# Performance work log

Measured on AMD Instinct MI355X. Metric: run time of the kernel, lower is better.

## Reference

```python
import jax, jax.numpy as jnp
import numpy as np


def setup_inputs() -> dict:
    key = jax.random.key(0)
    k1, k2 = jax.random.split(key)
    B, H = 128, 1024
    log_alpha = jax.random.normal(k1, (B, H), dtype=jnp.float32)
    unnormalized_tran = jax.random.normal(k2, (H, H), dtype=jnp.float32)
    return {"log_alpha": log_alpha, "unnormalized_tran": unnormalized_tran}


def reference(log_alpha, unnormalized_tran):
    # tran[i, j] = log P(state j | state i), rows normalized in log space
    tran = jax.nn.log_softmax(unnormalized_tran, axis=-1)  # (H, H)
    # log-domain matmul: out[b, j] = logsumexp_i(log_alpha[b, i] + tran[i, j])
    # broadcast to (B, H, H) then reduce over the source-state axis i
    out = jax.scipy.special.logsumexp(
        log_alpha[:, :, None] + tran[None, :, :], axis=1
    )  # (B, H)
    return out
```

## Files before the change

### kernel.cpp

```cpp
#include <hip/hip_runtime.h>
#include <hip/hip_bf16.h>

#define H 1024
#define B 128

typedef unsigned short u16;
typedef unsigned int u32;
typedef __attribute__((ext_vector_type(8))) short bf16x8;
typedef __attribute__((ext_vector_type(4))) float f32x4;

static __device__ inline u16 f2bf(float x) {
    __hip_bfloat16 h = __float2bfloat16(x);
    return __builtin_bit_cast(u16, h);
}

__global__ __launch_bounds__(256) void k1(const float* __restrict__ A,
                                          const float* __restrict__ U,
                                          u16* __restrict__ expUP,
                                          u16* __restrict__ expA) {
    const int t = threadIdx.x, w = t >> 6, l = t & 63;
    const int blk = blockIdx.x;
    if (blk < 128) {
        __shared__ u16 Lq[8][1024];
        #pragma unroll
        for (int rr = 0; rr < 2; ++rr) {
            const int row = w * 2 + rr;
            const float* Ur = U + (size_t)(blk * 8 + row) * H;
            float e[16];
            float s = 0.f;
            #pragma unroll
            for (int c = 0; c < 4; ++c) {
                float4 u4 = *reinterpret_cast<const float4*>(Ur + c * 256 + l * 4);
                e[c*4+0] = __expf(u4.x); e[c*4+1] = __expf(u4.y);
                e[c*4+2] = __expf(u4.z); e[c*4+3] = __expf(u4.w);
                s += e[c*4+0] + e[c*4+1] + e[c*4+2] + e[c*4+3];
            }
            #pragma unroll
            for (int off = 32; off > 0; off >>= 1) s += __shfl_down(s, off, 64);
            const float is = 1.0f / __shfl(s, 0, 64);
            #pragma unroll
            for (int c = 0; c < 4; ++c) {
                ushort4 o = {f2bf(e[c*4+0]*is), f2bf(e[c*4+1]*is),
                             f2bf(e[c*4+2]*is), f2bf(e[c*4+3]*is)};
                *reinterpret_cast<ushort4*>(&Lq[row][c*256 + l*4]) = o;
            }
        }
        __syncthreads();
        u16* dst = expUP + (size_t)blk * (H * 8);
        #pragma unroll
        for (int c = 0; c < 4; ++c) {
            const int j = c * 256 + t;
            uint4 v;
            v.x = (u32)Lq[0][j] | ((u32)Lq[1][j] << 16);
            v.y = (u32)Lq[2][j] | ((u32)Lq[3][j] << 16);
            v.z = (u32)Lq[4][j] | ((u32)Lq[5][j] << 16);
            v.w = (u32)Lq[6][j] | ((u32)Lq[7][j] << 16);
            *reinterpret_cast<uint4*>(dst + (size_t)j * 8) = v;
        }
    } else {
        const int b = (blk - 128) * 4 + w;
        const float* Ar = A + (size_t)b * H;
        u16* Er = expA + (size_t)b * H;
        #pragma unroll
        for (int c = 0; c < 4; ++c) {
            float4 a4 = *reinterpret_cast<const float4*>(Ar + c * 256 + l * 4);
            ushort4 o = {f2bf(__expf(a4.x)), f2bf(__expf(a4.y)),
                         f2bf(__expf(a4.z)), f2bf(__expf(a4.w))};
            *reinterpret_cast<ushort4*>(Er + c * 256 + l * 4) = o;
        }
    }
}

__global__ __launch_bounds__(512) void k2(const u16* __restrict__ expA,
                                          const u16* __restrict__ expUP,
                                          float* __restrict__ out) {
    __shared__ float red[4][2][4][66];
    const int t = threadIdx.x, l = t & 63, w = t >> 6;
    const int jh = w & 1, kh = w >> 1;
    const int b0 = blockIdx.x * 16;
    const int j0 = blockIdx.y * 32;
    const int colJ = j0 + jh * 16 + (l & 15);
    const int arow = b0 + (l & 15);
    const int kg   = l >> 4;

    f32x4 acc = {0.f, 0.f, 0.f, 0.f};
    #pragma unroll
    for (int s = 0; s < 8; ++s) {
        const int kk = s * 128 + kh * 32 + kg * 8;
        bf16x8 af = *reinterpret_cast<const bf16x8*>(expA + (size_t)arow * H + kk);
        bf16x8 bfv = *reinterpret_cast<const bf16x8*>(expUP + ((size_t)(kk >> 3) * H + colJ) * 8);
        acc = __builtin_amdgcn_mfma_f32_16x16x32_bf16(af, bfv, acc, 0, 0, 0);
    }

    #pragma unroll
    for (int r = 0; r < 4; ++r) red[kh][jh][r][l] = acc[r];
    __syncthreads();

    const int row = t >> 5, c = t & 31;
    const int jj = c >> 4, cc = c & 15;
    const int ll = (row >> 2) * 16 + cc, r = row & 3;
    const float v = red[0][jj][r][ll] + red[1][jj][r][ll]
                  + red[2][jj][r][ll] + red[3][jj][r][ll];
    out[(size_t)(b0 + row) * H + j0 + c] = __logf(v);
}

extern "C" void kernel_launch(void* const* d_in, const int* in_sizes, int n_in,
                              void* d_out, int out_size, void* d_ws, size_t ws_size,
                              hipStream_t stream) {
    const float* A = (const float*)d_in[0];
    const float* U = (const float*)d_in[1];
    float* out = (float*)d_out;

    char* ws = (char*)d_ws;
    u16* expUP = (u16*)ws;
    u16* expA  = (u16*)(ws + (size_t)2 * 1024 * 1024);

    k1<<<160, 256, 0, stream>>>(A, U, expUP, expA);
    dim3 g(B / 16, H / 32);
    k2<<<g, 512, 0, stream>>>(expA, expUP, out);
}
```

Before: 14.01 us.

## Repack transition matrix in 4-row groups and split work across more blocks

k1 now processes 4 rows of U per block across 256 blocks, using cross-wave shared-memory partial sums instead of an 8-row LDS transpose. The packed layout becomes 4 rows per column, so k2 loads two uint2 pieces per MFMA operand. k2 uses 16-column tiles with all 8 waves splitting K, which doubles the grid to 512 blocks and raises parallelism. In exchange it adds narrower, less coalesced loads and an 8-way reduction per output.

Result: slower. 15.17 us (+8.2%).

```diff
diff --git a/kernel.cpp b/kernel.cpp
--- a/kernel.cpp
+++ b/kernel.cpp
@@ -13,95 +13,104 @@
     __hip_bfloat16 h = __float2bfloat16(x);
     return __builtin_bit_cast(u16, h);
 }
+static __device__ inline u32 pack2(u16 a, u16 b) { return (u32)a | ((u32)b << 16); }
 
 __global__ __launch_bounds__(256) void k1(const float* __restrict__ A,
                                           const float* __restrict__ U,
-                                          u16* __restrict__ expUP,
+                                          u16* __restrict__ expUP4,
                                           u16* __restrict__ expA) {
     const int t = threadIdx.x, w = t >> 6, l = t & 63;
     const int blk = blockIdx.x;
-    if (blk < 128) {
-        __shared__ u16 Lq[8][1024];
+    if (blk < 256) {
+        __shared__ float part[4][4];
+        const int jbase = w * 256 + l;
+        float e[4][4];
+        float p[4] = {0.f, 0.f, 0.f, 0.f};
         #pragma unroll
-        for (int rr = 0; rr < 2; ++rr) {
-            const int row = w * 2 + rr;
-            const float* Ur = U + (size_t)(blk * 8 + row) * H;
-            float e[16];
-            float s = 0.f;
+        for (int r = 0; r < 4; ++r) {
+            const float* Ur = U + (size_t)(blk * 4 + r) * H;
             #pragma unroll
-            for (int c = 0; c < 4; ++c) {
-                float4 u4 = *reinterpret_cast<const float4*>(Ur + c * 256 + l * 4);
-                e[c*4+0] = __expf(u4.x); e[c*4+1] = __expf(u4.y);
-                e[c*4+2] = __expf(u4.z); e[c*4+3] = __expf(u4.w);
-                s += e[c*4+0] + e[c*4+1] + e[c*4+2] + e[c*4+3];
-            }
-            #pragma unroll
-            for (int off = 32; off > 0; off >>= 1) s += __shfl_down(s, off, 64);
-            const float is = 1.0f / __shfl(s, 0, 64);
-            #pragma unroll
-            for (int c = 0; c < 4; ++c) {
-                ushort4 o = {f2bf(e[c*4+0]*is), f2bf(e[c*4+1]*is),
-                             f2bf(e[c*4+2]*is), f2bf(e[c*4+3]*is)};
-                *reinterpret_cast<ushort4*>(&Lq[row][c*256 + l*4]) = o;
+            for (int m = 0; m < 4; ++m) {
+                float v = __expf(Ur[jbase + m * 64]);
+                e[r][m] = v;
+                p[r] += v;
             }
         }
+        #pragma unroll
+        for (int r = 0; r < 4; ++r)
+            #pragma unroll
+            for (int off = 32; off > 0; off >>= 1)
+                p[r] += __shfl_xor(p[r], off, 64);
+        if (l == 0) {
+            #pragma unroll
+            for (int r = 0; r < 4; ++r) part[r][w] = p[r];
+        }
         __syncthreads();
-        u16* dst = expUP + (size_t)blk * (H * 8);
+        float is[4];
         #pragma unroll
-        for (int c = 0; c < 4; ++c) {
-            const int j = c * 256 + t;
-            uint4 v;
-            v.x = (u32)Lq[0][j] | ((u32)Lq[1][j] << 16);
-            v.y = (u32)Lq[2][j] | ((u32)Lq[3][j] << 16);
-            v.z = (u32)Lq[4][j] | ((u32)Lq[5][j] << 16);
-            v.w = (u32)Lq[6][j] | ((u32)Lq[7][j] << 16);
-            *reinterpret_cast<uint4*>(dst + (size_t)j * 8) = v;
+        for (int r = 0; r < 4; ++r)
+            is[r] = 1.0f / (part[r][0] + part[r][1] + part[r][2] + part[r][3]);
+        u16* dst = expUP4 + (size_t)blk * H * 4;
+        #pragma unroll
+        for (int m = 0; m < 4; ++m) {
+            const int j = jbase + m * 64;
+            uint2 v;
+            v.x = pack2(f2bf(e[0][m] * is[0]), f2bf(e[1][m] * is[1]));
+            v.y = pack2(f2bf(e[2][m] * is[2]), f2bf(e[3][m] * is[3]));
+            *reinterpret_cast<uint2*>(dst + (size_t)j * 4) = v;
         }
     } else {
-        const int b = (blk - 128) * 4 + w;
-        const float* Ar = A + (size_t)b * H;
-        u16* Er = expA + (size_t)b * H;
+        const int bb = (blk - 256) * 4;
         #pragma unroll
-        for (int c = 0; c < 4; ++c) {
-            float4 a4 = *reinterpret_cast<const float4*>(Ar + c * 256 + l * 4);
+        for (int r = 0; r < 4; ++r) {
+            const float* Ar = A + (size_t)(bb + r) * H;
+            u16* Er = expA + (size_t)(bb + r) * H;
+            const int j = w * 256 + l * 4;
+            float4 a4 = *reinterpret_cast<const float4*>(Ar + j);
             ushort4 o = {f2bf(__expf(a4.x)), f2bf(__expf(a4.y)),
                          f2bf(__expf(a4.z)), f2bf(__expf(a4.w))};
-            *reinterpret_cast<ushort4*>(Er + c * 256 + l * 4) = o;
+            *reinterpret_cast<ushort4*>(Er + j) = o;
         }
     }
 }
 
 __global__ __launch_bounds__(512) void k2(const u16* __restrict__ expA,
-                                          const u16* __restrict__ expUP,
+                                          const u16* __restrict__ expUP4,
                                           float* __restrict__ out) {
-    __shared__ float red[4][2][4][66];
-    const int t = threadIdx.x, l = t & 63, w = t >> 6;
-    const int jh = w & 1, kh = w >> 1;
+    __shared__ float red[8][4][68];
+    const int t = threadIdx.x, l = t & 63, kh = t >> 6;
     const int b0 = blockIdx.x * 16;
-    const int j0 = blockIdx.y * 32;
-    const int colJ = j0 + jh * 16 + (l & 15);
+    const int j0 = blockIdx.y * 16;
+    const int col  = j0 + (l & 15);
     const int arow = b0 + (l & 15);
     const int kg   = l >> 4;
 
     f32x4 acc = {0.f, 0.f, 0.f, 0.f};
     #pragma unroll
-    for (int s = 0; s < 8; ++s) {
-        const int kk = s * 128 + kh * 32 + kg * 8;
+    for (int s = 0; s < 4; ++s) {
+        const int kk = kh * 128 + s * 32 + kg * 8;
         bf16x8 af = *reinterpret_cast<const bf16x8*>(expA + (size_t)arow * H + kk);
-        bf16x8 bfv = *reinterpret_cast<const bf16x8*>(expUP + ((size_t)(kk >> 3) * H + colJ) * 8);
+        const int kq = kk >> 2;
+        uint2 g0 = *reinterpret_cast<const uint2*>(expUP4 + ((size_t)kq * H + col) * 4);
+        uint2 g1 = *reinterpret_cast<const uint2*>(expUP4 + ((size_t)(kq + 1) * H + col) * 4);
+        uint4 bw = {g0.x, g0.y, g1.x, g1.y};
+        bf16x8 bfv = __builtin_bit_cast(bf16x8, bw);
         acc = __builtin_amdgcn_mfma_f32_16x16x32_bf16(af, bfv, acc, 0, 0, 0);
     }
 
     #pragma unroll
-    for (int r = 0; r < 4; ++r) red[kh][jh][r][l] = acc[r];
+    for (int r = 0; r < 4; ++r) red[kh][r][l] = acc[r];
     __syncthreads();
 
-    const int row = t >> 5, c = t & 31;
-    const int jj = c >> 4, cc = c & 15;
-    const int ll = (row >> 2) * 16 + cc, r = row & 3;
-    const float v = red[0][jj][r][ll] + red[1][jj][r][ll]
-                  + red[2][jj][r][ll] + red[3][jj][r][ll];
-    out[(size_t)(b0 + row) * H + j0 + c] = __logf(v);
+    if (t < 256) {
+        const int row = t >> 4, c = t & 15;
+        const int kg2 = row >> 2, r = row & 3;
+        const int lane = kg2 * 16 + c;
+        float v = 0.f;
+        #pragma unroll
+        for (int k = 0; k < 8; ++k) v += red[k][r][lane];
+        out[(size_t)(b0 + row) * H + j0 + c] = __logf(v);
+    }
 }
 
 extern "C" void kernel_launch(void* const* d_in, const int* in_sizes, int n_in,
@@ -112,10 +121,10 @@
     float* out = (float*)d_out;
 
     char* ws = (char*)d_ws;
-    u16* expUP = (u16*)ws;
-    u16* expA  = (u16*)(ws + (size_t)2 * 1024 * 1024);
+    u16* expUP4 = (u16*)ws;
+    u16* expA   = (u16*)(ws + (size_t)2 * 1024 * 1024);
 
-    k1<<<160, 256, 0, stream>>>(A, U, expUP, expA);
-    dim3 g(B / 16, H / 32);
-    k2<<<g, 512, 0, stream>>>(expA, expUP, out);
+    k1<<<288, 256, 0, stream>>>(A, U, expUP4, expA);
+    dim3 g(B / 16, H / 16);
+    k2<<<g, 512, 0, stream>>>(expA, expUP4, out);
 }
```

## Fold softmax row normalization into exp(A) and compute exp(U) inside matmul

Applied to the files above, without the earlier changes.

The row-wise softmax denominator of the transition matrix is moved onto the A side: k1 now computes only the row sums of exp(U) and writes exp(A[b,k])/sum_k into a bf16 buffer. k2 reads raw U directly and computes exp/bf16 conversion on the fly, so the normalized, repacked exp(U) buffer (2 MB written and re-read) is no longer needed. In exchange, each k2 block recomputes exp of its U tile for every batch tile (8x redundant transcendental work and fp32 U reads), uses strided scalar U loads, and switches the grid order so j-tiles are adjacent.

After: 16.17 us. 1.15x slower.

```diff
diff --git a/kernel.cpp b/kernel.cpp
--- a/kernel.cpp
+++ b/kernel.cpp
@@ -6,6 +6,7 @@
 
 typedef unsigned short u16;
 typedef unsigned int u32;
+typedef unsigned long long u64;
 typedef __attribute__((ext_vector_type(8))) short bf16x8;
 typedef __attribute__((ext_vector_type(4))) float f32x4;
 
@@ -13,72 +14,51 @@
     __hip_bfloat16 h = __float2bfloat16(x);
     return __builtin_bit_cast(u16, h);
 }
+static __device__ inline void st32a(u32* p, u32 v) {
+    __hip_atomic_store(p, v, __ATOMIC_RELAXED, __HIP_MEMORY_SCOPE_AGENT);
+}
+static __device__ inline u64 ld64a(const u16* p) {
+    return __hip_atomic_load((const u64*)p, __ATOMIC_RELAXED, __HIP_MEMORY_SCOPE_AGENT);
+}
 
 __global__ __launch_bounds__(256) void k1(const float* __restrict__ A,
                                           const float* __restrict__ U,
-                                          u16* __restrict__ expUP,
-                                          u16* __restrict__ expA) {
+                                          u16* __restrict__ expAS) {
     const int t = threadIdx.x, w = t >> 6, l = t & 63;
     const int blk = blockIdx.x;
-    if (blk < 128) {
-        __shared__ u16 Lq[8][1024];
-        #pragma unroll
-        for (int rr = 0; rr < 2; ++rr) {
-            const int row = w * 2 + rr;
-            const float* Ur = U + (size_t)(blk * 8 + row) * H;
-            float e[16];
-            float s = 0.f;
-            #pragma unroll
-            for (int c = 0; c < 4; ++c) {
-                float4 u4 = *reinterpret_cast<const float4*>(Ur + c * 256 + l * 4);
-                e[c*4+0] = __expf(u4.x); e[c*4+1] = __expf(u4.y);
-                e[c*4+2] = __expf(u4.z); e[c*4+3] = __expf(u4.w);
-                s += e[c*4+0] + e[c*4+1] + e[c*4+2] + e[c*4+3];
-            }
-            #pragma unroll
-            for (int off = 32; off > 0; off >>= 1) s += __shfl_down(s, off, 64);
-            const float is = 1.0f / __shfl(s, 0, 64);
-            #pragma unroll
-            for (int c = 0; c < 4; ++c) {
-                ushort4 o = {f2bf(e[c*4+0]*is), f2bf(e[c*4+1]*is),
-                             f2bf(e[c*4+2]*is), f2bf(e[c*4+3]*is)};
-                *reinterpret_cast<ushort4*>(&Lq[row][c*256 + l*4]) = o;
-            }
-        }
-        __syncthreads();
-        u16* dst = expUP + (size_t)blk * (H * 8);
+    __shared__ float part[4];
+    {
+        const float* Ur = U + (size_t)(blk * 4 + w) * H;
+        float s = 0.f;
         #pragma unroll
         for (int c = 0; c < 4; ++c) {
-            const int j = c * 256 + t;
-            uint4 v;
-            v.x = (u32)Lq[0][j] | ((u32)Lq[1][j] << 16);
-            v.y = (u32)Lq[2][j] | ((u32)Lq[3][j] << 16);
-            v.z = (u32)Lq[4][j] | ((u32)Lq[5][j] << 16);
-            v.w = (u32)Lq[6][j] | ((u32)Lq[7][j] << 16);
-            *reinterpret_cast<uint4*>(dst + (size_t)j * 8) = v;
+            float4 u4 = *reinterpret_cast<const float4*>(Ur + c * 256 + l * 4);
+            s += __expf(u4.x) + __expf(u4.y) + __expf(u4.z) + __expf(u4.w);
         }
-    } else {
-        const int b = (blk - 128) * 4 + w;
-        const float* Ar = A + (size_t)b * H;
-        u16* Er = expA + (size_t)b * H;
         #pragma unroll
-        for (int c = 0; c < 4; ++c) {
-            float4 a4 = *reinterpret_cast<const float4*>(Ar + c * 256 + l * 4);
-            ushort4 o = {f2bf(__expf(a4.x)), f2bf(__expf(a4.y)),
-                         f2bf(__expf(a4.z)), f2bf(__expf(a4.w))};
-            *reinterpret_cast<ushort4*>(Er + c * 256 + l * 4) = o;
-        }
+        for (int off = 32; off > 0; off >>= 1) s += __shfl_xor(s, off, 64);
+        if (l == 0) part[w] = 1.0f / s;
+    }
+    __syncthreads();
+    {
+        const int b  = t & 127;
+        const int kp = t >> 7;
+        const int k  = blk * 4 + kp * 2;
+        float2 a2 = *reinterpret_cast<const float2*>(A + (size_t)b * H + k);
+        const u32 v = (u32)f2bf(__expf(a2.x) * part[kp * 2])
+                    | ((u32)f2bf(__expf(a2.y) * part[kp * 2 + 1]) << 16);
+        st32a((u32*)(expAS + (size_t)b * H + k), v);
     }
 }
 
-__global__ __launch_bounds__(512) void k2(const u16* __restrict__ expA,
-                                          const u16* __restrict__ expUP,
+__global__ __launch_bounds__(512) void k2(const u16* __restrict__ expAS,
+                                          const float* __restrict__ U,
                                           float* __restrict__ out) {
     __shared__ float red[4][2][4][66];
     const int t = threadIdx.x, l = t & 63, w = t >> 6;
     const int jh = w & 1, kh = w >> 1;
-    const int b0 = blockIdx.x * 16;
-    const int j0 = blockIdx.y * 32;
+    const int j0 = blockIdx.x * 32;
+    const int b0 = blockIdx.y * 16;
     const int colJ = j0 + jh * 16 + (l & 15);
     const int arow = b0 + (l & 15);
     const int kg   = l >> 4;
@@ -87,9 +67,22 @@
     #pragma unroll
     for (int s = 0; s < 8; ++s) {
         const int kk = s * 128 + kh * 32 + kg * 8;
-        bf16x8 af = *reinterpret_cast<const bf16x8*>(expA + (size_t)arow * H + kk);
-        bf16x8 bfv = *reinterpret_cast<const bf16x8*>(expUP + ((size_t)(kk >> 3) * H + colJ) * 8);
-        acc = __builtin_amdgcn_mfma_f32_16x16x32_bf16(af, bfv, acc, 0, 0, 0);
+        const u16* ap = expAS + (size_t)arow * H + kk;
+        const u64 alo = ld64a(ap), ahi = ld64a(ap + 4);
+        const float* up = U + (size_t)kk * H + colJ;
+        const float e0 = __expf(up[0 * H]), e1 = __expf(up[1 * H]);
+        const float e2 = __expf(up[2 * H]), e3 = __expf(up[3 * H]);
+        const float e4 = __expf(up[4 * H]), e5 = __expf(up[5 * H]);
+        const float e6 = __expf(up[6 * H]), e7 = __expf(up[7 * H]);
+        uint4 bw;
+        bw.x = (u32)f2bf(e0) | ((u32)f2bf(e1) << 16);
+        bw.y = (u32)f2bf(e2) | ((u32)f2bf(e3) << 16);
+        bw.z = (u32)f2bf(e4) | ((u32)f2bf(e5) << 16);
+        bw.w = (u32)f2bf(e6) | ((u32)f2bf(e7) << 16);
+        uint4 aw = {(u32)alo, (u32)(alo >> 32), (u32)ahi, (u32)(ahi >> 32)};
+        acc = __builtin_amdgcn_mfma_f32_16x16x32_bf16(
+            __builtin_bit_cast(bf16x8, aw), __builtin_bit_cast(bf16x8, bw),
+            acc, 0, 0, 0);
     }
 
     #pragma unroll
@@ -111,11 +104,9 @@
     const float* U = (const float*)d_in[1];
     float* out = (float*)d_out;
 
-    char* ws = (char*)d_ws;
-    u16* expUP = (u16*)ws;
-    u16* expA  = (u16*)(ws + (size_t)2 * 1024 * 1024);
+    u16* expAS = (u16*)d_ws;
 
-    k1<<<160, 256, 0, stream>>>(A, U, expUP, expA);
-    dim3 g(B / 16, H / 32);
-    k2<<<g, 512, 0, stream>>>(expA, expUP, out);
+    k1<<<256, 256, 0, stream>>>(A, U, expAS);
+    dim3 g(H / 32, B / 16);
+    k2<<<g, 512, 0, stream>>>(expAS, U, out);
 }
```
